# Performance work log

Hardware: AMD Instinct MI355X
Metric: run time of the kernel (lower is better)

The kernel has to match this reference:

```python
import jax, jax.numpy as jnp
import numpy as np

B, S, D = 2, 2048, 256
QK, H, MLP = 256, 8, 1024
TOPK, R, MD = 8, 2048, 64
HD = QK // H
SCALE = HD ** -0.5
AVG_DEG = 32.0


def _layernorm(x, g, b, eps=1e-5):
    m = jnp.mean(x, axis=-1, keepdims=True)
    v = jnp.var(x, axis=-1, keepdims=True)
    return (x - m) * jax.lax.rsqrt(v + eps) * g + b


def _neighbor_mask(adj_matrix, region_memory, region_indices):
    # cluster neighbors: cosine-sim top-k over region memory, diagonal excluded
    nrm = jnp.linalg.norm(region_memory, axis=1, keepdims=True)
    nm = region_memory / (nrm + 1e-8)
    sim = nm @ nm.T                                   # [R, R]
    sim = jnp.where(jnp.eye(R, dtype=bool), -jnp.inf, sim)
    _, idx = jax.lax.top_k(sim, TOPK)                 # [R, TOPK]
    cmask = jnp.zeros((R, R), dtype=bool).at[jnp.arange(R)[:, None], idx].set(True)
    ext = adj_matrix | cmask                          # extended neighborhood [R, R]
    # token i attends to token positions j in neighborhood(region_indices[i]), j < S
    return ext[region_indices][:, :S]                 # [S, S] bool


def setup_inputs() -> dict:
    key = jax.random.key(0)
    ks = jax.random.split(key, 24)
    sc = 0.02
    inp = {
        "x": jax.random.normal(ks[0], (B, S, D), jnp.float32),
        "region_indices": jax.random.randint(ks[1], (S,), 0, R),
        "adj_matrix": jax.random.uniform(ks[2], (R, R)) < (AVG_DEG / R),
        "region_memory": jax.random.normal(ks[3], (R, MD), jnp.float32),
        # weights stored [in, out] (torch Linear is x @ W.T + b)
        "wq": jax.random.normal(ks[4], (D, QK)) * sc, "bq": jnp.zeros((QK,)),
        "wk": jax.random.normal(ks[5], (D, QK)) * sc, "bk": jnp.zeros((QK,)),
        "wv": jax.random.normal(ks[6], (D, QK)) * sc, "bv": jnp.zeros((QK,)),
        "wo": jax.random.normal(ks[7], (QK, D)) * sc, "bo": jnp.zeros((D,)),
        "ln1_g": jnp.ones((D,)), "ln1_b": jnp.zeros((D,)),
        "ln2_g": jnp.ones((D,)), "ln2_b": jnp.zeros((D,)),
        "gate_w": jax.random.normal(ks[8], (2 * D, D)) * sc, "gate_b": jnp.zeros((D,)),
        "ffn_w1": jax.random.normal(ks[9], (D, MLP)) * sc, "ffn_b1": jnp.zeros((MLP,)),
        "ffn_w2": jax.random.normal(ks[10], (MLP, D)) * sc, "ffn_b2": jnp.zeros((D,)),
    }
    return inp


def reference(x, region_indices, adj_matrix, region_memory,
              wq, bq, wk, bk, wv, bv, wo, bo,
              ln1_g, ln1_b, ln2_g, ln2_b,
              gate_w, gate_b, ffn_w1, ffn_b1, ffn_w2, ffn_b2):
    mask = _neighbor_mask(adj_matrix, region_memory, region_indices)  # [S, S]

    xn = _layernorm(x, ln1_g, ln1_b)
    q = (xn @ wq + bq).reshape(B, S, H, HD).transpose(0, 2, 1, 3)  # b h s d
    k = (xn @ wk + bk).reshape(B, S, H, HD).transpose(0, 2, 1, 3)
    v = (xn @ wv + bv).reshape(B, S, H, HD).transpose(0, 2, 1, 3)

    dots = jnp.einsum('bhid,bhjd->bhij', q, k) * SCALE
    # faithful to source: non-neighbor scores stay 0 (NOT -inf), softmax over all j
    scores = jnp.where(mask[None, None], dots, 0.0)
    attn = jax.nn.softmax(scores, axis=-1)
    out = jnp.einsum('bhij,bhjd->bhid', attn, v)
    out = out.transpose(0, 2, 1, 3).reshape(B, S, QK)
    attn_out = out @ wo + bo

    gate = jax.nn.sigmoid(jnp.concatenate([x, attn_out], axis=-1) @ gate_w + gate_b)
    fused = gate * x + (1.0 - gate) * attn_out

    h = _layernorm(fused, ln2_g, ln2_b)
    ffn_out = jax.nn.gelu(h @ ffn_w1 + ffn_b1, approximate=False) @ ffn_w2 + ffn_b2
    return fused + ffn_out
```

## Files before the change

kernel.cpp:

```cpp
#include <hip/hip_runtime.h>
#include <hip/hip_bf16.h>
#include <math.h>

#define B_ 2
#define S_ 2048
#define D_ 256
#define QK_ 256
#define H_ 8
#define HD_ 32
#define MLP_ 1024
#define TOPK_ 8
#define R_ 2048
#define MD_ 64
#define MAXN_ 192

using bf16_t = __hip_bfloat16;
using bf16x8 = __attribute__((ext_vector_type(8))) short;
using f32x4  = __attribute__((ext_vector_type(4))) float;

__device__ __constant__ float SCALE_ = 0.17677669529663687f;

__device__ inline float bf2f(short s) {
    union { unsigned int u; float f; } cvt;
    cvt.u = ((unsigned int)(unsigned short)s) << 16;
    return cvt.f;
}

__global__ void detect_adj(const unsigned int* __restrict__ adj, int* __restrict__ flag) {
    long g = (long)blockIdx.x * blockDim.x + threadIdx.x;
    long n = (long)R_ * R_ / 4;
    int found = 0;
    for (long i = g; i < n; i += (long)gridDim.x * blockDim.x) {
        if (adj[i] > 1u) { found = 1; break; }
    }
    if (found) atomicOr(flag, 1);
}

__device__ inline bool adj_on(const void* adj, int isbyte, long idx) {
    if (isbyte) return ((const unsigned char*)adj)[idx] != 0;
    return ((const int*)adj)[idx] != 0;
}

__global__ void norm_rm(const float* __restrict__ rm, bf16_t* __restrict__ nm_bf,
                        int* __restrict__ flag) {
    int r = blockIdx.x, t = threadIdx.x;
    if (r == 0 && t == 0) *flag = 0;
    float v = rm[r * MD_ + t];
    float s = v * v;
    for (int o = 32; o > 0; o >>= 1) s += __shfl_down(s, o);
    s = __shfl(s, 0);
    nm_bf[r * MD_ + t] = __float2bfloat16(v / (sqrtf(s) + 1e-8f));
}

__global__ __launch_bounds__(256) void topk_sel(const float* __restrict__ sim,
                                                int* __restrict__ tk) {
    int t = threadIdx.x;
    int w = t >> 6, ln = t & 63;
    int r = blockIdx.x * 4 + w;
    const float4* row4 = (const float4*)(sim + (long)r * R_);
    float4 f4[8];
#pragma unroll
    for (int k = 0; k < 8; k++) f4[k] = row4[ln + 64 * k];
    {
        int rem = (r >> 2) & 63, kw = r >> 8, jw = r & 3;
        if (rem == ln) {
#pragma unroll
            for (int k = 0; k < 8; k++)
                if (k == kw) {
                    if (jw == 0) f4[k].x = -INFINITY;
                    else if (jw == 1) f4[k].y = -INFINITY;
                    else if (jw == 2) f4[k].z = -INFINITY;
                    else f4[k].w = -INFINITY;
                }
        }
    }
    for (int it = 0; it < TOPK_; it++) {
        float bv = -INFINITY; int bi = 0x7fffffff;
#pragma unroll
        for (int k = 0; k < 8; k++) {
            int c0 = 4 * (ln + 64 * k);
            if (f4[k].x > bv) { bv = f4[k].x; bi = c0; }
            if (f4[k].y > bv) { bv = f4[k].y; bi = c0 + 1; }
            if (f4[k].z > bv) { bv = f4[k].z; bi = c0 + 2; }
            if (f4[k].w > bv) { bv = f4[k].w; bi = c0 + 3; }
        }
#pragma unroll
        for (int o = 32; o > 0; o >>= 1) {
            float ov = __shfl_down(bv, o); int oi = __shfl_down(bi, o);
            if (ov > bv || (ov == bv && oi < bi)) { bv = ov; bi = oi; }
        }
        int xi = __shfl(bi, 0);
        if (ln == 0) tk[r * TOPK_ + it] = xi;
        int rem = (xi >> 2) & 63, kw = xi >> 8, jw = xi & 3;
        if (rem == ln) {
#pragma unroll
            for (int k = 0; k < 8; k++)
                if (k == kw) {
                    if (jw == 0) f4[k].x = -INFINITY;
                    else if (jw == 1) f4[k].y = -INFINITY;
                    else if (jw == 2) f4[k].z = -INFINITY;
                    else f4[k].w = -INFINITY;
                }
        }
    }
}

__global__ __launch_bounds__(256) void build_nbr(const void* __restrict__ adj,
                                                 const int* __restrict__ tk,
                                                 const int* __restrict__ flag,
                                                 int* __restrict__ nbr_idx,
                                                 int* __restrict__ nbr_cnt) {
    __shared__ int cnt;
    int r = blockIdx.x, t = threadIdx.x;
    if (t == 0) cnt = 0;
    __syncthreads();
    int isbyte = *flag;
    for (int c = t; c < S_; c += 256) {
        long idx = (long)r * R_ + c;
        if (adj_on(adj, isbyte, idx)) {
            int p = atomicAdd(&cnt, 1);
            if (p < MAXN_) nbr_idx[r * MAXN_ + p] = c;
        }
    }
    __syncthreads();
    if (t < TOPK_) {
        int c = tk[r * TOPK_ + t];
        long idx = (long)r * R_ + c;
        if (!adj_on(adj, isbyte, idx) && c < S_) {
            int p = atomicAdd(&cnt, 1);
            if (p < MAXN_) nbr_idx[r * MAXN_ + p] = c;
        }
    }
    __syncthreads();
    if (t == 0) nbr_cnt[r] = min(cnt, MAXN_);
}

__global__ __launch_bounds__(256) void ln_kernel(const float* __restrict__ x,
                                                 const float* __restrict__ g,
                                                 const float* __restrict__ b,
                                                 bf16_t* __restrict__ y,
                                                 bf16_t* __restrict__ xcat) {
    __shared__ float red[256];
    int row = blockIdx.x, t = threadIdx.x;
    float v = x[(long)row * D_ + t];
    xcat[(long)row * 512 + t] = __float2bfloat16(v);
    red[t] = v; __syncthreads();
    for (int o = 128; o > 0; o >>= 1) { if (t < o) red[t] += red[t + o]; __syncthreads(); }
    float mean = red[0] / D_;
    __syncthreads();
    float dv = v - mean;
    red[t] = dv * dv; __syncthreads();
    for (int o = 128; o > 0; o >>= 1) { if (t < o) red[t] += red[t + o]; __syncthreads(); }
    float var = red[0] / D_;
    y[(long)row * D_ + t] = __float2bfloat16(dv * rsqrtf(var + 1e-5f) * g[t] + b[t]);
}

__global__ __launch_bounds__(256) void conv_w(const float* w0, const float* w1, const float* w2,
                                              const float* w3, const float* w4, const float* w5,
                                              const float* w6,
                                              const float* bq, const float* bk, const float* bv,
                                              bf16_t* wt, float* bqkv) {
    __shared__ float tile[32][33];
    int tb = blockIdx.x;
    if (tb >= 896) {
        int t = (tb - 896) * 256 + threadIdx.x;
        if (t < 768) bqkv[t] = t < 256 ? bq[t] : (t < 512 ? bk[t - 256] : bv[t - 512]);
        return;
    }
    const float* W; long dstoff; int K, N, local;
    if (tb < 64)       { W = w0; dstoff = 0;       K = 256;  N = 256;  local = tb; }
    else if (tb < 128) { W = w1; dstoff = 65536;   K = 256;  N = 256;  local = tb - 64; }
    else if (tb < 192) { W = w2; dstoff = 131072;  K = 256;  N = 256;  local = tb - 128; }
    else if (tb < 256) { W = w3; dstoff = 196608;  K = 256;  N = 256;  local = tb - 192; }
    else if (tb < 384) { W = w4; dstoff = 262144;  K = 512;  N = 256;  local = tb - 256; }
    else if (tb < 640) { W = w5; dstoff = 393216;  K = 256;  N = 1024; local = tb - 384; }
    else               { W = w6; dstoff = 655360;  K = 1024; N = 256;  local = tb - 640; }
    int ntn = N >> 5;
    int tk = local / ntn, tn = local - tk * ntn;
    int k0 = tk * 32, n0 = tn * 32;
    int r = threadIdx.x >> 5, c = threadIdx.x & 31;
#pragma unroll
    for (int rr = 0; rr < 4; rr++)
        tile[r + rr * 8][c] = W[(long)(k0 + r + rr * 8) * N + n0 + c];
    __syncthreads();
    bf16_t* dst = wt + dstoff;
#pragma unroll
    for (int rr = 0; rr < 4; rr++)
        dst[(long)(n0 + r + rr * 8) * K + k0 + c] = __float2bfloat16(tile[c][r + rr * 8]);
}

#define LDT64 72

template<int GELU>
__global__ __launch_bounds__(256) void mgemm64(const bf16_t* __restrict__ A,
                                               const bf16_t* __restrict__ Wt,
                                               const float* __restrict__ bias,
                                               const float* __restrict__ resid,
                                               float* __restrict__ Cf,
                                               bf16_t* __restrict__ Cb,
                                               int M, int N, int K, int ldcb) {
    __shared__ short As[64 * LDT64];
    __shared__ short Bs[64 * LDT64];
    int tid = threadIdx.x;
    int m0 = blockIdx.y * 64, n0 = blockIdx.x * 64;
    int w = tid >> 6, ln = tid & 63;
    int wr = w >> 1, wc = w & 1;
    int srow = tid >> 2, skb = (tid & 3) * 8;
    f32x4 zero4 = {0.f, 0.f, 0.f, 0.f};
    f32x4 acc[2][2];
#pragma unroll
    for (int i = 0; i < 2; i++)
#pragma unroll
        for (int j = 0; j < 2; j++) acc[i][j] = zero4;

    const bf16_t* Ab = A + (long)m0 * K + skb;
    const bf16_t* Bb = Wt + (long)n0 * K + skb;

    for (int k0 = 0; k0 < K; k0 += 64) {
        uint4 a0 = *(const uint4*)(Ab + (long)srow * K + k0);
        uint4 a1 = *(const uint4*)(Ab + (long)srow * K + k0 + 32);
        uint4 b0 = *(const uint4*)(Bb + (long)srow * K + k0);
        uint4 b1 = *(const uint4*)(Bb + (long)srow * K + k0 + 32);
        *(uint4*)(&As[srow * LDT64 + skb]) = a0;
        *(uint4*)(&As[srow * LDT64 + skb + 32]) = a1;
        *(uint4*)(&Bs[srow * LDT64 + skb]) = b0;
        *(uint4*)(&Bs[srow * LDT64 + skb + 32]) = b1;
        __syncthreads();
        int kr = (ln >> 4) * 8;
        int arow = wr * 32 + (ln & 15);
        int brow = wc * 32 + (ln & 15);
        bf16x8 af[2][2], bfr[2][2];
#pragma unroll
        for (int mi = 0; mi < 2; mi++)
#pragma unroll
            for (int ks = 0; ks < 2; ks++)
                af[mi][ks] = *(const bf16x8*)(&As[(arow + mi * 16) * LDT64 + ks * 32 + kr]);
#pragma unroll
        for (int ni = 0; ni < 2; ni++)
#pragma unroll
            for (int ks = 0; ks < 2; ks++)
                bfr[ni][ks] = *(const bf16x8*)(&Bs[(brow + ni * 16) * LDT64 + ks * 32 + kr]);
#pragma unroll
        for (int mi = 0; mi < 2; mi++)
#pragma unroll
            for (int ni = 0; ni < 2; ni++) {
                acc[mi][ni] = __builtin_amdgcn_mfma_f32_16x16x32_bf16(af[mi][0], bfr[ni][0], acc[mi][ni], 0, 0, 0);
                acc[mi][ni] = __builtin_amdgcn_mfma_f32_16x16x32_bf16(af[mi][1], bfr[ni][1], acc[mi][ni], 0, 0, 0);
            }
        __syncthreads();
    }
    int colb = n0 + wc * 32 + (ln & 15);
    int rowb = m0 + wr * 32 + (ln >> 4) * 4;
#pragma unroll
    for (int ni = 0; ni < 2; ni++) {
        int col = colb + ni * 16;
        float bv = bias ? bias[col] : 0.f;
#pragma unroll
        for (int mi = 0; mi < 2; mi++) {
#pragma unroll
            for (int r = 0; r < 4; r++) {
                int row = rowb + mi * 16 + r;
                float v = acc[mi][ni][r] + bv;
                if (GELU) v = 0.5f * v * (1.0f + erff(v * 0.70710678118654752f));
                if (resid) v += resid[(long)row * N + col];
                if (Cf) Cf[(long)row * N + col] = v;
                if (Cb) Cb[(long)row * ldcb + col] = __float2bfloat16(v);
            }
        }
    }
}

__global__ void vsum1(const bf16_t* __restrict__ qkv, float* __restrict__ part) {
    int b = blockIdx.x >> 6, ch = blockIdx.x & 63;
    int c = threadIdx.x;
    float s = 0.f;
    int j0 = ch * 32;
    for (int j = j0; j < j0 + 32; j++)
        s += __bfloat162float(qkv[((long)b * S_ + j) * 768 + 512 + c]);
    part[(long)blockIdx.x * QK_ + c] = s;
}

__global__ void vsum2(const float* __restrict__ part, float* __restrict__ vs) {
    int g = blockIdx.x * 256 + threadIdx.x;
    int b = g >> 8, c = g & 255;
    float s = 0.f;
    for (int ch = 0; ch < 64; ch++) s += part[(long)(b * 64 + ch) * QK_ + c];
    vs[g] = s;
}

__global__ __launch_bounds__(256) void attn_kernel(const bf16_t* __restrict__ qkv,
                                                   const float* __restrict__ vs,
                                                   const int* __restrict__ ridx,
                                                   const int* __restrict__ nbr_idx,
                                                   const int* __restrict__ nbr_cnt,
                                                   bf16_t* __restrict__ out) {
    __shared__ float qs[QK_];
    __shared__ float ej[H_][MAXN_];
    __shared__ int   nb[MAXN_];
    int bi = blockIdx.x;
    int b = bi >> 11, i = bi & (S_ - 1);
    int t = threadIdx.x;
    int h = t >> 5, ln = t & 31;
    int r = ridx[i];
    int cnt = nbr_cnt[r];
    qs[t] = __bfloat162float(qkv[(long)bi * 768 + t]);
    for (int p = t; p < cnt; p += 256) nb[p] = nbr_idx[r * MAXN_ + p];
    __syncthreads();
    const float* qh = qs + h * HD_;
    const bf16_t* kvb = qkv + (long)b * S_ * 768;
    float sreg[6];
    float lmax = 0.0f;
#pragma unroll
    for (int u = 0; u < 6; u++) {
        int p = ln + 32 * u;
        sreg[u] = 0.f;
        if (p < cnt) {
            int j = nb[p];
            const bf16x8* kr8 = (const bf16x8*)(kvb + (long)j * 768 + 256 + h * HD_);
            float s = 0.f;
#pragma unroll
            for (int q8 = 0; q8 < 4; q8++) {
                bf16x8 kk = kr8[q8];
#pragma unroll
                for (int e = 0; e < 8; e++)
                    s = fmaf(qh[q8 * 8 + e], bf2f(kk[e]), s);
            }
            s *= SCALE_;
            sreg[u] = s;
            lmax = fmaxf(lmax, s);
        }
    }
#pragma unroll
    for (int o = 16; o > 0; o >>= 1) lmax = fmaxf(lmax, __shfl_xor(lmax, o, 32));
    float lz = 0.f;
#pragma unroll
    for (int u = 0; u < 6; u++) {
        int p = ln + 32 * u;
        if (p < cnt) {
            float e = expf(sreg[u] - lmax);
            ej[h][p] = e;
            lz += e;
        }
    }
#pragma unroll
    for (int o = 16; o > 0; o >>= 1) lz += __shfl_xor(lz, o, 32);
    float em = expf(-lmax);
    float Z = lz + (float)(S_ - cnt) * em;
    float accv = 0.f, vn = 0.f;
    const bf16_t* vbase = kvb + 512 + h * HD_ + ln;
#pragma unroll 8
    for (int p = 0; p < cnt; p++) {
        int j = nb[p];
        float vv = __bfloat162float(vbase[(long)j * 768]);
        float e = ej[h][p];
        accv = fmaf(e, vv, accv);
        vn += vv;
    }
    float o = (em * (vs[b * QK_ + h * HD_ + ln] - vn) + accv) / Z;
    out[(long)bi * QK_ + h * HD_ + ln] = __float2bfloat16(o);
}

__global__ __launch_bounds__(256) void fuse_ln2_kernel(const float* __restrict__ x,
                                                       const float* __restrict__ ao,
                                                       const float* __restrict__ gp,
                                                       const float* __restrict__ g2,
                                                       const float* __restrict__ b2,
                                                       float* __restrict__ fused,
                                                       bf16_t* __restrict__ h) {
    __shared__ float red[256];
    int row = blockIdx.x, t = threadIdx.x;
    long idx = (long)row * D_ + t;
    float gate = 1.f / (1.f + expf(-gp[idx]));
    float f = gate * x[idx] + (1.f - gate) * ao[idx];
    fused[idx] = f;
    red[t] = f; __syncthreads();
    for (int o = 128; o > 0; o >>= 1) { if (t < o) red[t] += red[t + o]; __syncthreads(); }
    float mean = red[0] / D_;
    __syncthreads();
    float dv = f - mean;
    red[t] = dv * dv; __syncthreads();
    for (int o = 128; o > 0; o >>= 1) { if (t < o) red[t] += red[t + o]; __syncthreads(); }
    float var = red[0] / D_;
    h[idx] = __float2bfloat16(dv * rsqrtf(var + 1e-5f) * g2[t] + b2[t]);
}

extern "C" void kernel_launch(void* const* d_in, const int* in_sizes, int n_in,
                              void* d_out, int out_size, void* d_ws, size_t ws_size,
                              hipStream_t stream) {
    const float* x    = (const float*)d_in[0];
    const int*   ridx = (const int*)d_in[1];
    const void*  adj  = d_in[2];
    const float* rm   = (const float*)d_in[3];
    const float* wq = (const float*)d_in[4],  *bq = (const float*)d_in[5];
    const float* wk = (const float*)d_in[6],  *bk = (const float*)d_in[7];
    const float* wv = (const float*)d_in[8],  *bv = (const float*)d_in[9];
    const float* wo = (const float*)d_in[10], *bo = (const float*)d_in[11];
    const float* ln1g = (const float*)d_in[12], *ln1b = (const float*)d_in[13];
    const float* ln2g = (const float*)d_in[14], *ln2b = (const float*)d_in[15];
    const float* gw  = (const float*)d_in[16], *gb  = (const float*)d_in[17];
    const float* fw1 = (const float*)d_in[18], *fb1 = (const float*)d_in[19];
    const float* fw2 = (const float*)d_in[20], *fb2 = (const float*)d_in[21];
    float* out = (float*)d_out;

    float* wsf      = (float*)d_ws;
    int*   flag     = (int*)d_ws;
    bf16_t* nm_bf   = (bf16_t*)(wsf + 64);
    int*   tk       = (int*)(wsf + 64 + 131072);
    int*   nbr_idx  = tk + 16384;
    int*   nbr_cnt  = nbr_idx + R_ * MAXN_;
    bf16_t* qkv_bf  = (bf16_t*)(nbr_cnt + 2048);
    float* vs       = (float*)(nbr_cnt + 2048) + 3145728;
    float* gatep    = vs + 512;
    float* attn_out = gatep + 1048576;
    float* fusedb   = attn_out + 1048576;
    float* part     = fusedb + 1048576;
    bf16_t* xn_bf   = (bf16_t*)(part + 32768);
    bf16_t* attnO_bf= (bf16_t*)((float*)xn_bf + 524288);
    bf16_t* xcat_bf = (bf16_t*)((float*)attnO_bf + 524288);
    bf16_t* hb_bf   = (bf16_t*)((float*)xcat_bf + 1048576);
    bf16_t* f1_bf   = (bf16_t*)((float*)hb_bf + 524288);
    bf16_t* WT      = (bf16_t*)((float*)f1_bf + 2097152);
    float* bqkv     = (float*)WT + 458752;
    float* sim      = bqkv + 768;

    const int MROWS = B_ * S_;

    norm_rm<<<R_, 64, 0, stream>>>(rm, nm_bf, flag);
    detect_adj<<<256, 256, 0, stream>>>((const unsigned int*)adj, flag);

    mgemm64<0><<<dim3(R_ / 64, R_ / 64), 256, 0, stream>>>(
        nm_bf, nm_bf, nullptr, nullptr, sim, nullptr, R_, R_, MD_, 0);
    topk_sel<<<R_ / 4, 256, 0, stream>>>(sim, tk);

    build_nbr<<<R_, 256, 0, stream>>>(adj, tk, flag, nbr_idx, nbr_cnt);

    conv_w<<<899, 256, 0, stream>>>(wq, wk, wv, wo, gw, fw1, fw2, bq, bk, bv, WT, bqkv);

    ln_kernel<<<MROWS, 256, 0, stream>>>(x, ln1g, ln1b, xn_bf, xcat_bf);

    mgemm64<0><<<dim3(768 / 64, MROWS / 64), 256, 0, stream>>>(
        xn_bf, WT + 0, bqkv, nullptr, nullptr, qkv_bf, MROWS, 768, 256, 768);

    vsum1<<<B_ * 64, 256, 0, stream>>>(qkv_bf, part);
    vsum2<<<2, 256, 0, stream>>>(part, vs);
    attn_kernel<<<MROWS, 256, 0, stream>>>(qkv_bf, vs, ridx, nbr_idx, nbr_cnt, attnO_bf);

    mgemm64<0><<<dim3(256 / 64, MROWS / 64), 256, 0, stream>>>(
        attnO_bf, WT + 196608, bo, nullptr, attn_out, xcat_bf + 256, MROWS, 256, 256, 512);

    mgemm64<0><<<dim3(256 / 64, MROWS / 64), 256, 0, stream>>>(
        xcat_bf, WT + 262144, gb, nullptr, gatep, nullptr, MROWS, 256, 512, 0);

    fuse_ln2_kernel<<<MROWS, 256, 0, stream>>>(x, attn_out, gatep, ln2g, ln2b, fusedb, hb_bf);

    mgemm64<1><<<dim3(1024 / 64, MROWS / 64), 256, 0, stream>>>(
        hb_bf, WT + 393216, fb1, nullptr, nullptr, f1_bf, MROWS, 1024, 256, 1024);

    mgemm64<0><<<dim3(256 / 64, MROWS / 64), 256, 0, stream>>>(
        f1_bf, WT + 655360, fb2, fusedb, out, nullptr, MROWS, 256, 1024, 0);
}
```

Before: 136.5 us.

## Merge independent prologue kernels into horizontally fused mega-launches

Packs adjacency detection, region-memory normalization, weight transposition, bias packing and LayerNorm into one block-indexed launch. The sim GEMM, QKV GEMM (with a fused atomic V column-sum) and adjacency neighbor build go into a second launch, and top-k selection now appends directly to the neighbor lists via atomics. The aim is to cut launch count and serialization between small kernels and to drop the separate vsum passes. In exchange it adds float atomics whose order is nondeterministic, extra shared memory and register pressure in the mega-kernels, and a neighbor order that depends on atomics.

```diff
diff --git a/kernel.cpp b/kernel.cpp
--- a/kernel.cpp
+++ b/kernel.cpp
@@ -26,122 +26,162 @@
     return cvt.f;
 }
 
-__global__ void detect_adj(const unsigned int* __restrict__ adj, int* __restrict__ flag) {
-    long g = (long)blockIdx.x * blockDim.x + threadIdx.x;
-    long n = (long)R_ * R_ / 4;
-    int found = 0;
-    for (long i = g; i < n; i += (long)gridDim.x * blockDim.x) {
-        if (adj[i] > 1u) { found = 1; break; }
-    }
-    if (found) atomicOr(flag, 1);
-}
-
 __device__ inline bool adj_on(const void* adj, int isbyte, long idx) {
     if (isbyte) return ((const unsigned char*)adj)[idx] != 0;
     return ((const int*)adj)[idx] != 0;
 }
 
-__global__ void norm_rm(const float* __restrict__ rm, bf16_t* __restrict__ nm_bf,
-                        int* __restrict__ flag) {
-    int r = blockIdx.x, t = threadIdx.x;
-    if (r == 0 && t == 0) *flag = 0;
-    float v = rm[r * MD_ + t];
-    float s = v * v;
-    for (int o = 32; o > 0; o >>= 1) s += __shfl_down(s, o);
-    s = __shfl(s, 0);
-    nm_bf[r * MD_ + t] = __float2bfloat16(v / (sqrtf(s) + 1e-8f));
-}
-
-__global__ __launch_bounds__(256) void topk_sel(const float* __restrict__ sim,
-                                                int* __restrict__ tk) {
-    int t = threadIdx.x;
-    int w = t >> 6, ln = t & 63;
-    int r = blockIdx.x * 4 + w;
-    const float4* row4 = (const float4*)(sim + (long)r * R_);
-    float4 f4[8];
-#pragma unroll
-    for (int k = 0; k < 8; k++) f4[k] = row4[ln + 64 * k];
-    {
-        int rem = (r >> 2) & 63, kw = r >> 8, jw = r & 3;
-        if (rem == ln) {
-#pragma unroll
-            for (int k = 0; k < 8; k++)
-                if (k == kw) {
-                    if (jw == 0) f4[k].x = -INFINITY;
-                    else if (jw == 1) f4[k].y = -INFINITY;
-                    else if (jw == 2) f4[k].z = -INFINITY;
-                    else f4[k].w = -INFINITY;
-                }
-        }
-    }
-    for (int it = 0; it < TOPK_; it++) {
-        float bv = -INFINITY; int bi = 0x7fffffff;
-#pragma unroll
-        for (int k = 0; k < 8; k++) {
-            int c0 = 4 * (ln + 64 * k);
-            if (f4[k].x > bv) { bv = f4[k].x; bi = c0; }
-            if (f4[k].y > bv) { bv = f4[k].y; bi = c0 + 1; }
-            if (f4[k].z > bv) { bv = f4[k].z; bi = c0 + 2; }
-            if (f4[k].w > bv) { bv = f4[k].w; bi = c0 + 3; }
-        }
-#pragma unroll
-        for (int o = 32; o > 0; o >>= 1) {
-            float ov = __shfl_down(bv, o); int oi = __shfl_down(bi, o);
-            if (ov > bv || (ov == bv && oi < bi)) { bv = ov; bi = oi; }
-        }
-        int xi = __shfl(bi, 0);
-        if (ln == 0) tk[r * TOPK_ + it] = xi;
-        int rem = (xi >> 2) & 63, kw = xi >> 8, jw = xi & 3;
-        if (rem == ln) {
-#pragma unroll
-            for (int k = 0; k < 8; k++)
-                if (k == kw) {
-                    if (jw == 0) f4[k].x = -INFINITY;
-                    else if (jw == 1) f4[k].y = -INFINITY;
-                    else if (jw == 2) f4[k].z = -INFINITY;
-                    else f4[k].w = -INFINITY;
-                }
-        }
-    }
-}
-
-__global__ __launch_bounds__(256) void build_nbr(const void* __restrict__ adj,
-                                                 const int* __restrict__ tk,
-                                                 const int* __restrict__ flag,
-                                                 int* __restrict__ nbr_idx,
-                                                 int* __restrict__ nbr_cnt) {
-    __shared__ int cnt;
-    int r = blockIdx.x, t = threadIdx.x;
-    if (t == 0) cnt = 0;
-    __syncthreads();
-    int isbyte = *flag;
-    for (int c = t; c < S_; c += 256) {
-        long idx = (long)r * R_ + c;
-        if (adj_on(adj, isbyte, idx)) {
-            int p = atomicAdd(&cnt, 1);
-            if (p < MAXN_) nbr_idx[r * MAXN_ + p] = c;
-        }
-    }
-    __syncthreads();
-    if (t < TOPK_) {
-        int c = tk[r * TOPK_ + t];
-        long idx = (long)r * R_ + c;
-        if (!adj_on(adj, isbyte, idx) && c < S_) {
-            int p = atomicAdd(&cnt, 1);
-            if (p < MAXN_) nbr_idx[r * MAXN_ + p] = c;
-        }
-    }
-    __syncthreads();
-    if (t == 0) nbr_cnt[r] = min(cnt, MAXN_);
-}
-
-__global__ __launch_bounds__(256) void ln_kernel(const float* __restrict__ x,
-                                                 const float* __restrict__ g,
-                                                 const float* __restrict__ b,
-                                                 bf16_t* __restrict__ y,
-                                                 bf16_t* __restrict__ xcat) {
+#define LDT64 72
+
+__device__ __forceinline__ void gemm_tile(const bf16_t* __restrict__ A, int lda,
+                                          const bf16_t* __restrict__ Bt, int ldb,
+                                          const float* __restrict__ bias,
+                                          const float* __restrict__ resid,
+                                          float* __restrict__ Cf,
+                                          bf16_t* __restrict__ Cb, int ldcb,
+                                          float* __restrict__ vsat,
+                                          int N, int K, int mt, int nt, int gelu,
+                                          int tid, short* As, short* Bs) {
+    int m0 = mt * 64, n0 = nt * 64;
+    int w = tid >> 6, ln = tid & 63;
+    int wr = w >> 1, wc = w & 1;
+    int srow = tid >> 2, skb = (tid & 3) * 8;
+    f32x4 zero4 = {0.f, 0.f, 0.f, 0.f};
+    f32x4 acc[2][2];
+#pragma unroll
+    for (int i = 0; i < 2; i++)
+#pragma unroll
+        for (int j = 0; j < 2; j++) acc[i][j] = zero4;
+
+    const bf16_t* Ab = A + (long)m0 * lda + skb;
+    const bf16_t* Bb = Bt + (long)n0 * ldb + skb;
+
+    for (int k0 = 0; k0 < K; k0 += 64) {
+        uint4 a0 = *(const uint4*)(Ab + (long)srow * lda + k0);
+        uint4 a1 = *(const uint4*)(Ab + (long)srow * lda + k0 + 32);
+        uint4 b0 = *(const uint4*)(Bb + (long)srow * ldb + k0);
+        uint4 b1 = *(const uint4*)(Bb + (long)srow * ldb + k0 + 32);
+        *(uint4*)(&As[srow * LDT64 + skb]) = a0;
+        *(uint4*)(&As[srow * LDT64 + skb + 32]) = a1;
+        *(uint4*)(&Bs[srow * LDT64 + skb]) = b0;
+        *(uint4*)(&Bs[srow * LDT64 + skb + 32]) = b1;
+        __syncthreads();
+        int kr = (ln >> 4) * 8;
+        int arow = wr * 32 + (ln & 15);
+        int brow = wc * 32 + (ln & 15);
+        bf16x8 af[2][2], bfr[2][2];
+#pragma unroll
+        for (int mi = 0; mi < 2; mi++)
+#pragma unroll
+            for (int ks = 0; ks < 2; ks++)
+                af[mi][ks] = *(const bf16x8*)(&As[(arow + mi * 16) * LDT64 + ks * 32 + kr]);
+#pragma unroll
+        for (int ni = 0; ni < 2; ni++)
+#pragma unroll
+            for (int ks = 0; ks < 2; ks++)
+                bfr[ni][ks] = *(const bf16x8*)(&Bs[(brow + ni * 16) * LDT64 + ks * 32 + kr]);
+#pragma unroll
+        for (int mi = 0; mi < 2; mi++)
+#pragma unroll
+            for (int ni = 0; ni < 2; ni++) {
+                acc[mi][ni] = __builtin_amdgcn_mfma_f32_16x16x32_bf16(af[mi][0], bfr[ni][0], acc[mi][ni], 0, 0, 0);
+                acc[mi][ni] = __builtin_amdgcn_mfma_f32_16x16x32_bf16(af[mi][1], bfr[ni][1], acc[mi][ni], 0, 0, 0);
+            }
+        __syncthreads();
+    }
+    int colb = n0 + wc * 32 + (ln & 15);
+    int rowb = m0 + wr * 32 + (ln >> 4) * 4;
+#pragma unroll
+    for (int ni = 0; ni < 2; ni++) {
+        int col = colb + ni * 16;
+        float bv = bias ? bias[col] : 0.f;
+        float vcol = 0.f;
+#pragma unroll
+        for (int mi = 0; mi < 2; mi++) {
+#pragma unroll
+            for (int r = 0; r < 4; r++) {
+                int row = rowb + mi * 16 + r;
+                float v = acc[mi][ni][r] + bv;
+                if (gelu) v = 0.5f * v * (1.0f + erff(v * 0.70710678118654752f));
+                if (resid) v += resid[(long)row * N + col];
+                if (Cf) Cf[(long)row * N + col] = v;
+                if (Cb) Cb[(long)row * ldcb + col] = __float2bfloat16(v);
+                vcol += v;
+            }
+        }
+        if (vsat && col >= 512)
+            atomicAdd(&vsat[((m0 >> 11) << 8) + (col - 512)], vcol);
+    }
+}
+
+__global__ __launch_bounds__(256) void mega1(const unsigned int* __restrict__ adjw,
+                                             int* __restrict__ flag,
+                                             const float* __restrict__ rm, bf16_t* __restrict__ nm_bf,
+                                             const float* __restrict__ x,
+                                             const float* __restrict__ ln1g, const float* __restrict__ ln1b,
+                                             bf16_t* __restrict__ xn_bf, bf16_t* __restrict__ xcat,
+                                             const float* w0, const float* w1, const float* w2,
+                                             const float* w3, const float* w4, const float* w5,
+                                             const float* w6,
+                                             const float* bq, const float* bk, const float* bv,
+                                             bf16_t* __restrict__ wt, float* __restrict__ bqkv,
+                                             float* __restrict__ vs) {
+    __shared__ float tile[32][33];
     __shared__ float red[256];
-    int row = blockIdx.x, t = threadIdx.x;
+    int tb = blockIdx.x, t = threadIdx.x;
+    if (tb < 256) {
+        long g = (long)tb * 256 + t;
+        long n = (long)R_ * R_ / 4;
+        int found = 0;
+        for (long i = g; i < n; i += 65536)
+            if (adjw[i] > 1u) { found = 1; break; }
+        if (found) atomicOr(flag, 1);
+        return;
+    }
+    if (tb < 768) {
+        int w = t >> 6, ln = t & 63;
+        int r = (tb - 256) * 4 + w;
+        float v = rm[r * MD_ + ln];
+        float s = v * v;
+        for (int o = 32; o > 0; o >>= 1) s += __shfl_down(s, o);
+        s = __shfl(s, 0);
+        nm_bf[r * MD_ + ln] = __float2bfloat16(v / (sqrtf(s) + 1e-8f));
+        return;
+    }
+    if (tb < 1667) {
+        int cb = tb - 768;
+        if (cb >= 896) {
+            int tt = (cb - 896) * 256 + t;
+            if (tt < 768) bqkv[tt] = tt < 256 ? bq[tt] : (tt < 512 ? bk[tt - 256] : bv[tt - 512]);
+            return;
+        }
+        const float* W; long dstoff; int K, N, local;
+        if (cb < 64)       { W = w0; dstoff = 0;       K = 256;  N = 256;  local = cb; }
+        else if (cb < 128) { W = w1; dstoff = 65536;   K = 256;  N = 256;  local = cb - 64; }
+        else if (cb < 192) { W = w2; dstoff = 131072;  K = 256;  N = 256;  local = cb - 128; }
+        else if (cb < 256) { W = w3; dstoff = 196608;  K = 256;  N = 256;  local = cb - 192; }
+        else if (cb < 384) { W = w4; dstoff = 262144;  K = 512;  N = 256;  local = cb - 256; }
+        else if (cb < 640) { W = w5; dstoff = 393216;  K = 256;  N = 1024; local = cb - 384; }
+        else               { W = w6; dstoff = 655360;  K = 1024; N = 256;  local = cb - 640; }
+        int ntn = N >> 5;
+        int tk2 = local / ntn, tn = local - tk2 * ntn;
+        int k0 = tk2 * 32, n0 = tn * 32;
+        int r = t >> 5, c = t & 31;
+#pragma unroll
+        for (int rr = 0; rr < 4; rr++)
+            tile[r + rr * 8][c] = W[(long)(k0 + r + rr * 8) * N + n0 + c];
+        __syncthreads();
+        bf16_t* dst = wt + dstoff;
+#pragma unroll
+        for (int rr = 0; rr < 4; rr++)
+            dst[(long)(n0 + r + rr * 8) * K + k0 + c] = __float2bfloat16(tile[c][r + rr * 8]);
+        return;
+    }
+    if (tb == 1667) {
+        vs[t] = 0.f; vs[t + 256] = 0.f;
+        return;
+    }
+    int row = tb - 1668;
     float v = x[(long)row * D_ + t];
     xcat[(long)row * 512 + t] = __float2bfloat16(v);
     red[t] = v; __syncthreads();
@@ -152,140 +192,123 @@
     red[t] = dv * dv; __syncthreads();
     for (int o = 128; o > 0; o >>= 1) { if (t < o) red[t] += red[t + o]; __syncthreads(); }
     float var = red[0] / D_;
-    y[(long)row * D_ + t] = __float2bfloat16(dv * rsqrtf(var + 1e-5f) * g[t] + b[t]);
-}
-
-__global__ __launch_bounds__(256) void conv_w(const float* w0, const float* w1, const float* w2,
-                                              const float* w3, const float* w4, const float* w5,
-                                              const float* w6,
-                                              const float* bq, const float* bk, const float* bv,
-                                              bf16_t* wt, float* bqkv) {
-    __shared__ float tile[32][33];
-    int tb = blockIdx.x;
-    if (tb >= 896) {
-        int t = (tb - 896) * 256 + threadIdx.x;
-        if (t < 768) bqkv[t] = t < 256 ? bq[t] : (t < 512 ? bk[t - 256] : bv[t - 512]);
-        return;
-    }
-    const float* W; long dstoff; int K, N, local;
-    if (tb < 64)       { W = w0; dstoff = 0;       K = 256;  N = 256;  local = tb; }
-    else if (tb < 128) { W = w1; dstoff = 65536;   K = 256;  N = 256;  local = tb - 64; }
-    else if (tb < 192) { W = w2; dstoff = 131072;  K = 256;  N = 256;  local = tb - 128; }
-    else if (tb < 256) { W = w3; dstoff = 196608;  K = 256;  N = 256;  local = tb - 192; }
-    else if (tb < 384) { W = w4; dstoff = 262144;  K = 512;  N = 256;  local = tb - 256; }
-    else if (tb < 640) { W = w5; dstoff = 393216;  K = 256;  N = 1024; local = tb - 384; }
-    else               { W = w6; dstoff = 655360;  K = 1024; N = 256;  local = tb - 640; }
-    int ntn = N >> 5;
-    int tk = local / ntn, tn = local - tk * ntn;
-    int k0 = tk * 32, n0 = tn * 32;
-    int r = threadIdx.x >> 5, c = threadIdx.x & 31;
-#pragma unroll
-    for (int rr = 0; rr < 4; rr++)
-        tile[r + rr * 8][c] = W[(long)(k0 + r + rr * 8) * N + n0 + c];
+    xn_bf[(long)row * D_ + t] = __float2bfloat16(dv * rsqrtf(var + 1e-5f) * ln1g[t] + ln1b[t]);
+}
+
+__global__ __launch_bounds__(256) void mega2(const bf16_t* __restrict__ nm_bf, float* __restrict__ sim,
+                                             const bf16_t* __restrict__ xn_bf,
+                                             const bf16_t* __restrict__ WT, const float* __restrict__ bqkv,
+                                             bf16_t* __restrict__ qkv_bf, float* __restrict__ vs,
+                                             const void* __restrict__ adj, const int* __restrict__ flag,
+                                             int* __restrict__ nbr_idx, int* __restrict__ nbr_cnt) {
+    __shared__ short As[64 * LDT64];
+    __shared__ short Bs[64 * LDT64];
+    int tb = blockIdx.x, t = threadIdx.x;
+    if (tb < 1024) {
+        gemm_tile(nm_bf, 64, nm_bf, 64, nullptr, nullptr, sim, nullptr, 0, nullptr,
+                  2048, 64, tb >> 5, tb & 31, 0, t, As, Bs);
+        return;
+    }
+    if (tb < 1792) {
+        int local = tb - 1024;
+        gemm_tile(xn_bf, 256, WT, 256, bqkv, nullptr, nullptr, qkv_bf, 768, vs,
+                  768, 256, local / 12, local % 12, 0, t, As, Bs);
+        return;
+    }
+    __shared__ int cnt;
+    int r = tb - 1792;
+    if (t == 0) cnt = 0;
     __syncthreads();
-    bf16_t* dst = wt + dstoff;
-#pragma unroll
-    for (int rr = 0; rr < 4; rr++)
-        dst[(long)(n0 + r + rr * 8) * K + k0 + c] = __float2bfloat16(tile[c][r + rr * 8]);
-}
-
-#define LDT64 72
+    int isbyte = *flag;
+    for (int c = t; c < S_; c += 256) {
+        long idx = (long)r * R_ + c;
+        if (adj_on(adj, isbyte, idx)) {
+            int p = atomicAdd(&cnt, 1);
+            if (p < MAXN_) nbr_idx[r * MAXN_ + p] = c;
+        }
+    }
+    __syncthreads();
+    if (t == 0) nbr_cnt[r] = cnt;
+}
+
+__global__ __launch_bounds__(256) void topk_append(const float* __restrict__ sim,
+                                                   const void* __restrict__ adj,
+                                                   const int* __restrict__ flag,
+                                                   int* __restrict__ nbr_idx,
+                                                   int* __restrict__ nbr_cnt) {
+    int t = threadIdx.x;
+    int w = t >> 6, ln = t & 63;
+    int r = blockIdx.x * 4 + w;
+    const float4* row4 = (const float4*)(sim + (long)r * R_);
+    float4 f4[8];
+#pragma unroll
+    for (int k = 0; k < 8; k++) f4[k] = row4[ln + 64 * k];
+    {
+        int rem = (r >> 2) & 63, kw = r >> 8, jw = r & 3;
+        if (rem == ln) {
+#pragma unroll
+            for (int k = 0; k < 8; k++)
+                if (k == kw) {
+                    if (jw == 0) f4[k].x = -INFINITY;
+                    else if (jw == 1) f4[k].y = -INFINITY;
+                    else if (jw == 2) f4[k].z = -INFINITY;
+                    else f4[k].w = -INFINITY;
+                }
+        }
+    }
+    int myc = 0x7fffffff;
+#pragma unroll
+    for (int it = 0; it < TOPK_; it++) {
+        float bv = -INFINITY; int bi = 0x7fffffff;
+#pragma unroll
+        for (int k = 0; k < 8; k++) {
+            int c0 = 4 * (ln + 64 * k);
+            if (f4[k].x > bv) { bv = f4[k].x; bi = c0; }
+            if (f4[k].y > bv) { bv = f4[k].y; bi = c0 + 1; }
+            if (f4[k].z > bv) { bv = f4[k].z; bi = c0 + 2; }
+            if (f4[k].w > bv) { bv = f4[k].w; bi = c0 + 3; }
+        }
+#pragma unroll
+        for (int o = 32; o > 0; o >>= 1) {
+            float ov = __shfl_down(bv, o); int oi = __shfl_down(bi, o);
+            if (ov > bv || (ov == bv && oi < bi)) { bv = ov; bi = oi; }
+        }
+        int xi = __shfl(bi, 0);
+        if (ln == it) myc = xi;
+        int rem = (xi >> 2) & 63, kw = xi >> 8, jw = xi & 3;
+        if (rem == ln) {
+#pragma unroll
+            for (int k = 0; k < 8; k++)
+                if (k == kw) {
+                    if (jw == 0) f4[k].x = -INFINITY;
+                    else if (jw == 1) f4[k].y = -INFINITY;
+                    else if (jw == 2) f4[k].z = -INFINITY;
+                    else f4[k].w = -INFINITY;
+                }
+        }
+    }
+    if (ln < TOPK_) {
+        int isbyte = *flag;
+        int c = myc;
+        if (c < S_ && !adj_on(adj, isbyte, (long)r * R_ + c)) {
+            int p = atomicAdd(&nbr_cnt[r], 1);
+            if (p < MAXN_) nbr_idx[r * MAXN_ + p] = c;
+        }
+    }
+}
 
 template<int GELU>
-__global__ __launch_bounds__(256) void mgemm64(const bf16_t* __restrict__ A,
-                                               const bf16_t* __restrict__ Wt,
+__global__ __launch_bounds__(256) void mgemm64(const bf16_t* __restrict__ A, int lda,
+                                               const bf16_t* __restrict__ Wt, int ldb,
                                                const float* __restrict__ bias,
                                                const float* __restrict__ resid,
                                                float* __restrict__ Cf,
-                                               bf16_t* __restrict__ Cb,
-                                               int M, int N, int K, int ldcb) {
+                                               bf16_t* __restrict__ Cb, int ldcb,
+                                               int N, int K) {
     __shared__ short As[64 * LDT64];
     __shared__ short Bs[64 * LDT64];
-    int tid = threadIdx.x;
-    int m0 = blockIdx.y * 64, n0 = blockIdx.x * 64;
-    int w = tid >> 6, ln = tid & 63;
-    int wr = w >> 1, wc = w & 1;
-    int srow = tid >> 2, skb = (tid & 3) * 8;
-    f32x4 zero4 = {0.f, 0.f, 0.f, 0.f};
-    f32x4 acc[2][2];
-#pragma unroll
-    for (int i = 0; i < 2; i++)
-#pragma unroll
-        for (int j = 0; j < 2; j++) acc[i][j] = zero4;
-
-    const bf16_t* Ab = A + (long)m0 * K + skb;
-    const bf16_t* Bb = Wt + (long)n0 * K + skb;
-
-    for (int k0 = 0; k0 < K; k0 += 64) {
-        uint4 a0 = *(const uint4*)(Ab + (long)srow * K + k0);
-        uint4 a1 = *(const uint4*)(Ab + (long)srow * K + k0 + 32);
-        uint4 b0 = *(const uint4*)(Bb + (long)srow * K + k0);
-        uint4 b1 = *(const uint4*)(Bb + (long)srow * K + k0 + 32);
-        *(uint4*)(&As[srow * LDT64 + skb]) = a0;
-        *(uint4*)(&As[srow * LDT64 + skb + 32]) = a1;
-        *(uint4*)(&Bs[srow * LDT64 + skb]) = b0;
-        *(uint4*)(&Bs[srow * LDT64 + skb + 32]) = b1;
-        __syncthreads();
-        int kr = (ln >> 4) * 8;
-        int arow = wr * 32 + (ln & 15);
-        int brow = wc * 32 + (ln & 15);
-        bf16x8 af[2][2], bfr[2][2];
-#pragma unroll
-        for (int mi = 0; mi < 2; mi++)
-#pragma unroll
-            for (int ks = 0; ks < 2; ks++)
-                af[mi][ks] = *(const bf16x8*)(&As[(arow + mi * 16) * LDT64 + ks * 32 + kr]);
-#pragma unroll
-        for (int ni = 0; ni < 2; ni++)
-#pragma unroll
-            for (int ks = 0; ks < 2; ks++)
-                bfr[ni][ks] = *(const bf16x8*)(&Bs[(brow + ni * 16) * LDT64 + ks * 32 + kr]);
-#pragma unroll
-        for (int mi = 0; mi < 2; mi++)
-#pragma unroll
-            for (int ni = 0; ni < 2; ni++) {
-                acc[mi][ni] = __builtin_amdgcn_mfma_f32_16x16x32_bf16(af[mi][0], bfr[ni][0], acc[mi][ni], 0, 0, 0);
-                acc[mi][ni] = __builtin_amdgcn_mfma_f32_16x16x32_bf16(af[mi][1], bfr[ni][1], acc[mi][ni], 0, 0, 0);
-            }
-        __syncthreads();
-    }
-    int colb = n0 + wc * 32 + (ln & 15);
-    int rowb = m0 + wr * 32 + (ln >> 4) * 4;
-#pragma unroll
-    for (int ni = 0; ni < 2; ni++) {
-        int col = colb + ni * 16;
-        float bv = bias ? bias[col] : 0.f;
-#pragma unroll
-        for (int mi = 0; mi < 2; mi++) {
-#pragma unroll
-            for (int r = 0; r < 4; r++) {
-                int row = rowb + mi * 16 + r;
-                float v = acc[mi][ni][r] + bv;
-                if (GELU) v = 0.5f * v * (1.0f + erff(v * 0.70710678118654752f));
-                if (resid) v += resid[(long)row * N + col];
-                if (Cf) Cf[(long)row * N + col] = v;
-                if (Cb) Cb[(long)row * ldcb + col] = __float2bfloat16(v);
-            }
-        }
-    }
-}
-
-__global__ void vsum1(const bf16_t* __restrict__ qkv, float* __restrict__ part) {
-    int b = blockIdx.x >> 6, ch = blockIdx.x & 63;
-    int c = threadIdx.x;
-    float s = 0.f;
-    int j0 = ch * 32;
-    for (int j = j0; j < j0 + 32; j++)
-        s += __bfloat162float(qkv[((long)b * S_ + j) * 768 + 512 + c]);
-    part[(long)blockIdx.x * QK_ + c] = s;
-}
-
-__global__ void vsum2(const float* __restrict__ part, float* __restrict__ vs) {
-    int g = blockIdx.x * 256 + threadIdx.x;
-    int b = g >> 8, c = g & 255;
-    float s = 0.f;
-    for (int ch = 0; ch < 64; ch++) s += part[(long)(b * 64 + ch) * QK_ + c];
-    vs[g] = s;
+    gemm_tile(A, lda, Wt, ldb, bias, resid, Cf, Cb, ldcb, nullptr,
+              N, K, blockIdx.y, blockIdx.x, GELU, threadIdx.x, As, Bs);
 }
 
 __global__ __launch_bounds__(256) void attn_kernel(const bf16_t* __restrict__ qkv,
@@ -302,7 +325,7 @@
     int t = threadIdx.x;
     int h = t >> 5, ln = t & 31;
     int r = ridx[i];
-    int cnt = nbr_cnt[r];
+    int cnt = min(nbr_cnt[r], MAXN_);
     qs[t] = __bfloat162float(qkv[(long)bi * 768 + t]);
     for (int p = t; p < cnt; p += 256) nb[p] = nbr_idx[r * MAXN_ + p];
     __syncthreads();
@@ -405,8 +428,7 @@
     float* wsf      = (float*)d_ws;
     int*   flag     = (int*)d_ws;
     bf16_t* nm_bf   = (bf16_t*)(wsf + 64);
-    int*   tk       = (int*)(wsf + 64 + 131072);
-    int*   nbr_idx  = tk + 16384;
+    int*   nbr_idx  = (int*)(wsf + 64 + 131072 + 16384);
     int*   nbr_cnt  = nbr_idx + R_ * MAXN_;
     bf16_t* qkv_bf  = (bf16_t*)(nbr_cnt + 2048);
     float* vs       = (float*)(nbr_cnt + 2048) + 3145728;
@@ -425,37 +447,30 @@
 
     const int MROWS = B_ * S_;
 
-    norm_rm<<<R_, 64, 0, stream>>>(rm, nm_bf, flag);
-    detect_adj<<<256, 256, 0, stream>>>((const unsigned int*)adj, flag);
-
-    mgemm64<0><<<dim3(R_ / 64, R_ / 64), 256, 0, stream>>>(
-        nm_bf, nm_bf, nullptr, nullptr, sim, nullptr, R_, R_, MD_, 0);
-    topk_sel<<<R_ / 4, 256, 0, stream>>>(sim, tk);
-
-    build_nbr<<<R_, 256, 0, stream>>>(adj, tk, flag, nbr_idx, nbr_cnt);
-
-    conv_w<<<899, 256, 0, stream>>>(wq, wk, wv, wo, gw, fw1, fw2, bq, bk, bv, WT, bqkv);
-
-    ln_kernel<<<MROWS, 256, 0, stream>>>(x, ln1g, ln1b, xn_bf, xcat_bf);
-
-    mgemm64<0><<<dim3(768 / 64, MROWS / 64), 256, 0, stream>>>(
-        xn_bf, WT + 0, bqkv, nullptr, nullptr, qkv_bf, MROWS, 768, 256, 768);
-
-    vsum1<<<B_ * 64, 256, 0, stream>>>(qkv_bf, part);
-    vsum2<<<2, 256, 0, stream>>>(part, vs);
+    hipMemsetAsync(flag, 0, sizeof(int), stream);
+
+    mega1<<<5764, 256, 0, stream>>>(
+        (const unsigned int*)adj, flag, rm, nm_bf, x, ln1g, ln1b, xn_bf, xcat_bf,
+        wq, wk, wv, wo, gw, fw1, fw2, bq, bk, bv, WT, bqkv, vs);
+
+    mega2<<<3840, 256, 0, stream>>>(
+        nm_bf, sim, xn_bf, WT, bqkv, qkv_bf, vs, adj, flag, nbr_idx, nbr_cnt);
+
+    topk_append<<<R_ / 4, 256, 0, stream>>>(sim, adj, flag, nbr_idx, nbr_cnt);
+
     attn_kernel<<<MROWS, 256, 0, stream>>>(qkv_bf, vs, ridx, nbr_idx, nbr_cnt, attnO_bf);
 
     mgemm64<0><<<dim3(256 / 64, MROWS / 64), 256, 0, stream>>>(
-        attnO_bf, WT + 196608, bo, nullptr, attn_out, xcat_bf + 256, MROWS, 256, 256, 512);
+        attnO_bf, 256, WT + 196608, 256, bo, nullptr, attn_out, xcat_bf + 256, 512, 256, 256);
 
     mgemm64<0><<<dim3(256 / 64, MROWS / 64), 256, 0, stream>>>(
-        xcat_bf, WT + 262144, gb, nullptr, gatep, nullptr, MROWS, 256, 512, 0);
+        xcat_bf, 512, WT + 262144, 512, gb, nullptr, gatep, nullptr, 0, 256, 512);
 
     fuse_ln2_kernel<<<MROWS, 256, 0, stream>>>(x, attn_out, gatep, ln2g, ln2b, fusedb, hb_bf);
 
     mgemm64<1><<<dim3(1024 / 64, MROWS / 64), 256, 0, stream>>>(
-        hb_bf, WT + 393216, fb1, nullptr, nullptr, f1_bf, MROWS, 1024, 256, 1024);
+        hb_bf, 256, WT + 393216, 256, fb1, nullptr, nullptr, f1_bf, 1024, 1024, 256);
 
     mgemm64<0><<<dim3(256 / 64, MROWS / 64), 256, 0, stream>>>(
-        f1_bf, WT + 655360, fb2, fusedb, out, nullptr, MROWS, 256, 1024, 0);
-}
+        f1_bf, 1024, WT + 655360, 1024, fb2, fusedb, out, nullptr, 0, 256, 1024);
+}
```

Measured after the change: 140.0 us. 2.6% more time.
